# Kernel optimization log

Measured on AMD Instinct MI355X. Metric: run time of the kernel, lower is better.

The kernel has to match this reference:

```python
import jax, jax.numpy as jnp
import numpy as np

GROUPS = 4
BN_EPS = 1e-5


def conv2d(x, w, pad=0):
    return jax.lax.conv_general_dilated(x, w, (1, 1), [(pad, pad), (pad, pad)],
                                        dimension_numbers=('NCHW', 'OIHW', 'NCHW'))


def bn_infer(x, g, b, m, v):
    s = g * jax.lax.rsqrt(v + BN_EPS)
    return x * s[None, :, None, None] + (b - m * s)[None, :, None, None]


def refine_residual(x, w1, w3a, g, b, m, v, w3b):
    # RefineResidual(has_relu=True): 1x1 -> ConvBnRelu(3x3) -> 3x3 conv, residual, relu
    x1 = conv2d(x, w1)
    t = jax.nn.relu(bn_infer(conv2d(x1, w3a, pad=1), g, b, m, v))
    t = conv2d(t, w3b, pad=1)
    return jax.nn.relu(t + x1)


def grid_edges(H, W):
    # 4-connected pixel grid: right + down neighbors
    idx = np.arange(H * W).reshape(H, W)
    eu = np.concatenate([idx[:, :-1].ravel(), idx[:-1, :].ravel()]).astype(np.int32)
    ev = np.concatenate([idx[:, 1:].ravel(), idx[1:, :].ravel()]).astype(np.int32)
    return jnp.asarray(eu), jnp.asarray(ev)


def boruvka_mst(w, eu, ev, N):
    # Boruvka MST over the grid graph; returns bool mask over edges (N-1 True).
    E = w.shape[0]
    nodes = jnp.arange(N, dtype=jnp.int32)
    order = jnp.argsort(w).astype(jnp.int32)                  # edge ids by weight (unique ranks)
    rank = jnp.zeros(E, jnp.int32).at[order].set(jnp.arange(E, dtype=jnp.int32))
    BIG = jnp.int32(E)
    R = int(np.ceil(np.log2(max(N, 2)))) + 2

    def flatten(p):
        return jax.lax.fori_loop(0, R, lambda _, q: q[q], p)

    def body(_, state):
        parent, mst = state
        cu, cv = parent[eu], parent[ev]
        key = jnp.where(cu != cv, rank, BIG)
        cmin = jnp.minimum(jax.ops.segment_min(key, cu, num_segments=N),
                           jax.ops.segment_min(key, cv, num_segments=N))
        valid = cmin < BIG
        e = order[jnp.minimum(cmin, E - 1)]                   # min outgoing edge per component
        mst = mst.at[e].max(valid)
        other = jnp.where(cu[e] == nodes, cv[e], cu[e])
        pnew = jnp.where(valid, other, nodes)
        # break mutual (2-cycle) merges: smaller label becomes root
        pnew = jnp.where((pnew[pnew] == nodes) & (nodes < pnew), nodes, pnew)
        return flatten(pnew), mst

    _, mst = jax.lax.fori_loop(0, R + 2, body, (nodes, jnp.zeros(E, bool)))
    return mst


def root_and_depth(mst, eu, ev, N):
    # BFS-root the tree at node 0 -> parent pointers, then depth by pointer doubling.
    pn = jnp.full(N, -1, jnp.int32).at[0].set(0)

    def bfs(_, pn):
        vis = pn >= 0
        a = mst & vis[eu] & (~vis[ev])
        b = mst & vis[ev] & (~vis[eu])
        pn = pn.at[ev].max(jnp.where(a, eu, jnp.int32(-1)))
        pn = pn.at[eu].max(jnp.where(b, ev, jnp.int32(-1)))
        return pn

    pn = jax.lax.fori_loop(0, N, bfs, pn)
    R = int(np.ceil(np.log2(max(N, 2)))) + 2
    d0 = (jnp.arange(N) != 0).astype(jnp.int32)

    def dbl(_, s):
        d, p = s
        return d + d[p], p[p]

    depth, _ = jax.lax.fori_loop(0, R, dbl, (d0, pn))
    return pn, depth


def tree_filter_group(x, w, pn, depth):
    # Exact O(N) two-pass tree filter: y_i = sum_j prod(path weights i->j) x_j.
    # x: [N, C] (ones channel appended by caller), w: [N] edge weight to parent.
    N = x.shape[0]
    notroot = jnp.arange(N) != 0

    def up(i, agg):                                           # leaves -> root
        lev = N - 1 - i
        sel = (depth == lev) & notroot
        return agg.at[pn].add(jnp.where(sel[:, None], w[:, None] * agg, 0.0))

    agg = jax.lax.fori_loop(0, N - 1, up, x)

    def down(lev, F):                                         # root -> leaves
        cand = agg + w[:, None] * (F[pn] - w[:, None] * agg)
        return jnp.where(((depth == lev) & notroot)[:, None], cand, F)

    return jax.lax.fori_loop(1, N, down, agg)


def tree_filter_2d(feat, emb, pn, depth):
    # Grouped normalized tree filtering (TreeFilter2D): per-group edge affinity
    # exp(-||e_v - e_parent(v)||^2); normalize by filtering an all-ones channel.
    B, C, H, W = feat.shape
    N = H * W
    f = feat.reshape(B, GROUPS, C // GROUPS, N)
    e = emb.reshape(B, GROUPS, -1, N)

    def per_batch(fb, eb, pnb, db):
        w = jnp.exp(-jnp.sum((eb - eb[:, :, pnb]) ** 2, axis=1))   # [G, N]
        x = jnp.concatenate([fb, jnp.ones_like(fb[:, :1])], axis=1)
        x = jnp.swapaxes(x, 1, 2)                                  # [G, N, Cg+1]
        out = jax.vmap(lambda xg, wg: tree_filter_group(xg, wg, pnb, db))(x, w)
        y = out[..., :-1] / out[..., -1:]
        return jnp.swapaxes(y, 1, 2)

    out = jax.vmap(per_batch)(f, e, pn, depth)
    return out.reshape(B, C, H, W)


def _forward(fm, last_fm, lat_w1, lat_w3a, lat_g, lat_b, lat_m, lat_v, lat_w3b,
             ref_w1, ref_w3a, ref_g, ref_b, ref_m, ref_v, ref_w3b, emb_w):
    B, Cb, H, W = fm.shape
    N = H * W
    eu, ev = grid_edges(H, W)
    latent = refine_residual(fm, lat_w1, lat_w3a, lat_g, lat_b, lat_m, lat_v, lat_w3b)
    # MinimumSpanningTree(norm2_distance) on backbone features fm
    f = fm.reshape(B, Cb, N)
    dist = jnp.sum((f[:, :, eu] - f[:, :, ev]) ** 2, axis=1)       # [B, E]
    mst = jax.vmap(lambda d: boruvka_mst(d, eu, ev, N))(dist)
    pn, depth = jax.vmap(lambda m: root_and_depth(m, eu, ev, N))(mst)
    embed = conv2d(last_fm, emb_w)                                 # embed_layer (1x1, no bn/relu)
    fusion = latent + tree_filter_2d(last_fm, embed, pn, depth)
    return refine_residual(fusion, ref_w1, ref_w3a, ref_g, ref_b, ref_m, ref_v, ref_w3b)


def setup_inputs() -> dict:
    key = jax.random.key(0)
    ks = jax.random.split(key, 12)
    B, Cb, Cbiz, Cemb, H, W = 2, 1024, 64, 32, 32, 32
    r = lambda k, s: jax.random.normal(k, s, jnp.float32) * 0.05
    return dict(
        fm=jax.random.normal(ks[0], (B, Cb, H, W), jnp.float32),
        last_fm=jax.random.normal(ks[1], (B, Cbiz, H, W), jnp.float32),
        lat_w1=r(ks[2], (Cbiz, Cb, 1, 1)),
        lat_w3a=r(ks[3], (Cbiz, Cbiz, 3, 3)),
        lat_g=jnp.ones(Cbiz, jnp.float32),
        lat_b=jnp.zeros(Cbiz, jnp.float32),
        lat_m=jnp.zeros(Cbiz, jnp.float32),
        lat_v=jax.random.uniform(ks[4], (Cbiz,), jnp.float32, 0.5, 1.5),
        lat_w3b=r(ks[5], (Cbiz, Cbiz, 3, 3)),
        ref_w1=r(ks[6], (Cbiz, Cbiz, 1, 1)),
        ref_w3a=r(ks[7], (Cbiz, Cbiz, 3, 3)),
        ref_g=jnp.ones(Cbiz, jnp.float32),
        ref_b=jnp.zeros(Cbiz, jnp.float32),
        ref_m=jnp.zeros(Cbiz, jnp.float32),
        ref_v=jax.random.uniform(ks[8], (Cbiz,), jnp.float32, 0.5, 1.5),
        ref_w3b=r(ks[9], (Cbiz, Cbiz, 3, 3)),
        emb_w=r(ks[10], (Cemb, Cbiz, 1, 1)),
    )


def reference(fm, last_fm, lat_w1, lat_w3a, lat_g, lat_b, lat_m, lat_v, lat_w3b,
              ref_w1, ref_w3a, ref_g, ref_b, ref_m, ref_v, ref_w3b, emb_w):
    return _forward(fm, last_fm, lat_w1, lat_w3a, lat_g, lat_b, lat_m, lat_v, lat_w3b,
                    ref_w1, ref_w3a, ref_g, ref_b, ref_m, ref_v, ref_w3b, emb_w)
```

## Files before the change

kernel.cpp:

```cpp
#include <hip/hip_runtime.h>
#include <hip/hip_bf16.h>

#define NN 1024
#define EE 1984

__device__ __forceinline__ void edge_uv(int e, int* u, int* v) {
    if (e < 992) {
        int r = e / 31, c = e - r * 31;
        *u = r * 32 + c; *v = *u + 1;
    } else {
        *u = e - 992; *v = *u + 32;
    }
}

__device__ void conv1x1_tile(const float* __restrict__ in, const float* __restrict__ in2,
                             const float* __restrict__ w,
                             float* __restrict__ out, int CIN, int Cout,
                             int b, int co0, int n0, float* red) {
    int tid = threadIdx.x;
    int px = tid & 63, kc = tid >> 6;
    int kcu = __builtin_amdgcn_readfirstlane(kc);
    int KCH = CIN >> 4;
    size_t ibase = (size_t)b * CIN * NN + n0 + px;
    const float* wr = w + (size_t)co0 * CIN;
    float acc[8] = {0.f,0.f,0.f,0.f,0.f,0.f,0.f,0.f};
    for (int ci = kcu * KCH; ci < kcu * KCH + KCH; ++ci) {
        float xv = in[ibase + (size_t)ci * NN];
        if (in2) xv += in2[ibase + (size_t)ci * NN];
#pragma unroll
        for (int j = 0; j < 8; ++j)
            acc[j] += wr[j * CIN + ci] * xv;
    }
#pragma unroll
    for (int j = 0; j < 8; ++j) red[j * 1024 + tid] = acc[j];
    __syncthreads();
    for (int s = 8; s >= 1; s >>= 1) {
        if (kc < s) {
#pragma unroll
            for (int j = 0; j < 8; ++j)
                red[j * 1024 + kc * 64 + px] += red[j * 1024 + (kc + s) * 64 + px];
        }
        __syncthreads();
    }
    if (kc == 0) {
        size_t ob = ((size_t)b * Cout + co0) * NN + n0 + px;
#pragma unroll
        for (int j = 0; j < 8; ++j) out[ob + (size_t)j * NN] = red[j * 1024 + px];
    }
}

__device__ void dist_tile(const float* __restrict__ fm, float* __restrict__ dist,
                          int b, int eb, float* red) {
    int tid = threadIdx.x;
    int le = tid & 63, kc = tid >> 6;
    int kcu = __builtin_amdgcn_readfirstlane(kc);
    int e = eb * 64 + le;
    int u, v; edge_uv(e, &u, &v);
    const float* fp = fm + (size_t)b * 1024 * NN;
    float s = 0.f;
    for (int c = kcu * 64; c < kcu * 64 + 64; ++c) {
        float d = fp[(size_t)c * NN + u] - fp[(size_t)c * NN + v];
        s += d * d;
    }
    red[tid] = s;
    __syncthreads();
    for (int ss = 8; ss >= 1; ss >>= 1) {
        if (kc < ss) red[kc * 64 + le] += red[(kc + ss) * 64 + le];
        __syncthreads();
    }
    if (kc == 0) dist[b * EE + e] = red[le];
}

__device__ void conv3x3_body(const float* __restrict__ in, const float* __restrict__ w,
                             const float* __restrict__ gg, const float* __restrict__ bb,
                             const float* __restrict__ mm, const float* __restrict__ vv,
                             const float* __restrict__ res, float* __restrict__ out,
                             int mode, int b, int co, int r0, float* pl) {
    int tid = threadIdx.x;
    const float* ip = in + (size_t)b * 64 * NN;
    const float* wp = w + (size_t)co * 64 * 9;
    int r = tid >> 5, c = tid & 31;
    float acc = 0.f;
    for (int h = 0; h < 2; ++h) {
        __syncthreads();
        for (int i4 = tid; i4 < 32 * 80; i4 += 256) {
            int ci = i4 / 80, o = i4 - ci * 80;
            int row = r0 - 1 + (o >> 3), c4 = (o & 7) << 2;
            float4 val = make_float4(0.f, 0.f, 0.f, 0.f);
            if (row >= 0 && row < 32)
                val = *(const float4*)&ip[(size_t)(h * 32 + ci) * NN + row * 32 + c4];
            *(float4*)&pl[ci * 320 + (o >> 3) * 32 + c4] = val;
        }
        __syncthreads();
        for (int ci = 0; ci < 32; ++ci) {
            float wv[9];
#pragma unroll
            for (int q = 0; q < 9; ++q) wv[q] = wp[(h * 32 + ci) * 9 + q];
            float s = 0.f;
#pragma unroll
            for (int dy = 0; dy < 3; ++dy) {
                const float* row = &pl[ci * 320 + (r + dy) * 32];
#pragma unroll
                for (int dx = -1; dx <= 1; ++dx) {
                    int cc = c + dx;
                    float xv = (cc >= 0 && cc < 32) ? row[cc] : 0.f;
                    s += wv[dy * 3 + (dx + 1)] * xv;
                }
            }
            acc += s;
        }
    }
    float val;
    size_t op = ((size_t)b * 64 + co) * NN + r0 * 32 + tid;
    if (mode == 0) {
        float sc = gg[co] * rsqrtf(vv[co] + 1e-5f);
        val = acc * sc + (bb[co] - mm[co] * sc);
    } else {
        val = acc + res[op];
    }
    out[op] = fmaxf(val, 0.f);
}

struct MstS {
    unsigned long long minkey[NN];
    unsigned long long ekey[EE];
    int parent[NN], pnw[NN], pn[NN], dep[NN], scr[NN], elist[NN];
    int mstm[EE];
    int cnt, cnt2;
};

__device__ void mst_body_1024(const float* __restrict__ dist, int b, MstS* S,
                              int* __restrict__ pn_g, int* __restrict__ maxd_g,
                              int* __restrict__ ord_g, int* __restrict__ off_g) {
    int tid = threadIdx.x;
    const float* wb = dist + b * EE;
    S->parent[tid] = tid;
    for (int e = tid; e < EE; e += 1024) {
        S->mstm[e] = 0;
        S->ekey[e] = ((unsigned long long)__float_as_uint(wb[e]) << 32) | (unsigned)e;
    }
    if (tid == 0) { S->cnt = 0; S->cnt2 = 0; }
    __syncthreads();

    for (int round = 0; round < 14; ++round) {
        S->minkey[tid] = ~0ULL;
        __syncthreads();
        for (int e = tid; e < EE; e += 1024) {
            int u, v; edge_uv(e, &u, &v);
            int cu = S->parent[u], cv = S->parent[v];
            if (cu != cv) {
                unsigned long long k = S->ekey[e];
                atomicMin(&S->minkey[cu], k);
                atomicMin(&S->minkey[cv], k);
            }
        }
        __syncthreads();
        int np;
        unsigned long long mk = S->minkey[tid];
        if (mk != ~0ULL) {
            int e = (int)(mk & 0xffffffffULL);
            if (atomicExch(&S->mstm[e], 1) == 0) atomicAdd(&S->cnt, 1);
            int eu, ev; edge_uv(e, &eu, &ev);
            int cu = S->parent[eu], cv = S->parent[ev];
            np = (cu == tid) ? cv : cu;
        } else np = tid;
        S->pnw[tid] = np;
        __syncthreads();
        int q = S->pnw[tid];
        int pq = S->pnw[q];
        S->parent[tid] = (pq == tid && tid < q) ? tid : q;
        for (;;) {
            int ch = 0;
            int p = S->parent[tid];
            int pp = S->parent[p];
            if (pp != p) { S->parent[tid] = pp; ch = 1; }
            if (!__syncthreads_or(ch)) break;
        }
        if (S->cnt == NN - 1) break;
    }

    for (int e = tid; e < EE; e += 1024)
        if (S->mstm[e]) { int s = atomicAdd(&S->cnt2, 1); S->elist[s] = e; }
    __syncthreads();
    int ecnt = S->cnt2;

    S->pn[tid] = (tid == 0) ? 0 : -1;
    __syncthreads();
    volatile int* vpn = S->pn;
    int myu = 0, myv = 0; bool have = tid < ecnt;
    if (have) { edge_uv(S->elist[tid], &myu, &myv); }
    for (;;) {
        int ch = 0;
        for (int s = 0; s < 8; ++s) {
            if (have) {
                int pu = vpn[myu], pv = vpn[myv];
                if (pu >= 0 && pv < 0)      { vpn[myv] = myu; ch = 1; }
                else if (pv >= 0 && pu < 0) { vpn[myu] = myv; ch = 1; }
            }
        }
        if (!__syncthreads_or(ch)) break;
    }

    S->dep[tid] = (tid != 0) ? 1 : 0;
    S->pnw[tid] = S->pn[tid];
    __syncthreads();
    int* dA = S->dep; int* dB = S->scr; int* pA = S->pnw; int* pB = S->parent;
    for (int it = 0; it < 12; ++it) {
        int p = pA[tid];
        int j = (p < 0) ? (NN + p) : p;
        int nd = dA[tid] + dA[j];
        int np2 = pA[j];
        __syncthreads();
        dB[tid] = nd; pB[tid] = np2;
        __syncthreads();
        int* t = dA; dA = dB; dB = t;
        t = pA; pA = pB; pB = t;
    }
    if (tid == 0) S->cnt = 0;
    __syncthreads();
    int d = S->dep[tid];
    if (d >= 1 && d <= NN - 1) atomicMax(&S->cnt, d);
    __syncthreads();
    int maxd = S->cnt;

    S->scr[tid] = 0;
    __syncthreads();
    int bkt = (tid != 0 && d >= 1 && d <= NN - 1) ? d : 0;
    atomicAdd(&S->scr[bkt], 1);
    __syncthreads();
    int cntv = S->scr[tid];
    int lane = tid & 63, wid = tid >> 6;
    int x = cntv;
    for (int d2 = 1; d2 < 64; d2 <<= 1) {
        int y = __shfl_up(x, d2, 64);
        if (lane >= d2) x += y;
    }
    if (lane == 63) S->pnw[wid] = x;
    __syncthreads();
    if (tid < 16) {
        int off = 0;
        for (int i = 0; i < tid; ++i) off += S->pnw[i];
        S->parent[tid] = off;
    }
    __syncthreads();
    int excl = x - cntv + S->parent[wid];
    int* mi = (int*)S->minkey;
    mi[tid] = excl;
    S->scr[tid] = excl;
    __syncthreads();
    int pos = atomicAdd(&S->scr[bkt], 1);
    S->elist[pos] = tid;
    __syncthreads();

    pn_g[b * NN + tid]    = S->pn[tid];
    ord_g[b * NN + tid]   = S->elist[tid];
    off_g[b * 1025 + tid] = mi[tid];
    if (tid == 0) { off_g[b * 1025 + 1024] = NN; maxd_g[b] = maxd; }
}

struct TfSmem { float agg[NN * 3]; float wv[NN]; int jj[NN]; int ords[NN]; int offs[1025]; };
__device__ void treefilter_wave(const float* __restrict__ feat, const float* __restrict__ emb,
                                const int* __restrict__ pn_g, const int* __restrict__ ord_g,
                                const int* __restrict__ off_g, const int* __restrict__ maxd_g,
                                float* __restrict__ tfout, int b, int g, int sub, TfSmem* S) {
    int lane = threadIdx.x;
    const float* eb = emb + ((size_t)b * 32 + g * 8) * NN;
    int c0 = g * 16 + sub * 2;
    const float* fb = feat + ((size_t)b * 64 + c0) * NN;
    for (int k = 0; k < 16; ++k) {
        int v = lane + k * 64;
        int p = pn_g[b * NN + v];
        int j = (p < 0) ? (NN + p) : p;
        S->jj[v] = j;
        float s = 0.f;
#pragma unroll
        for (int q = 0; q < 8; ++q) {
            float d = eb[(size_t)q * NN + v] - eb[(size_t)q * NN + j];
            s += d * d;
        }
        S->wv[v] = expf(-s);
        S->agg[v * 3 + 0] = fb[v];
        S->agg[v * 3 + 1] = fb[NN + v];
        S->agg[v * 3 + 2] = 1.f;
        S->ords[v] = ord_g[b * NN + v];
        S->offs[v] = off_g[b * 1025 + v];
    }
    if (lane == 0) S->offs[1024] = NN;
    int maxdep = maxd_g[b];
    for (int lev = maxdep; lev >= 1; --lev) {
        int s0 = S->offs[lev], s1 = S->offs[lev + 1];
        for (int i = s0 + lane; i < s1; i += 64) {
            int v = S->ords[i]; int j = S->jj[v]; float w = S->wv[v];
            atomicAdd(&S->agg[j * 3 + 0], w * S->agg[v * 3 + 0]);
            atomicAdd(&S->agg[j * 3 + 1], w * S->agg[v * 3 + 1]);
            atomicAdd(&S->agg[j * 3 + 2], w * S->agg[v * 3 + 2]);
        }
    }
    for (int lev = 1; lev <= maxdep; ++lev) {
        int s0 = S->offs[lev], s1 = S->offs[lev + 1];
        for (int i = s0 + lane; i < s1; i += 64) {
            int v = S->ords[i]; int j = S->jj[v]; float w = S->wv[v];
#pragma unroll
            for (int c = 0; c < 3; ++c) {
                float a = S->agg[v * 3 + c];
                S->agg[v * 3 + c] = a + w * (S->agg[j * 3 + c] - w * a);
            }
        }
    }
    float* ob = tfout + ((size_t)b * 64 + c0) * NN;
    for (int k = 0; k < 16; ++k) {
        int v = lane + k * 64;
        float inv = 1.f / S->agg[v * 3 + 2];
        ob[v]      = S->agg[v * 3 + 0] * inv;
        ob[NN + v] = S->agg[v * 3 + 1] * inv;
    }
}

__global__ __launch_bounds__(1024) void k0_dist(
    const float* __restrict__ fm, float* __restrict__ dist) {
    __shared__ float red[1024];
    int i = blockIdx.x;
    dist_tile(fm, dist, i / 31, i % 31, red);
}

union K1S { float red[8192]; MstS m; };
__global__ __launch_bounds__(1024) void k1_fused(
    const float* __restrict__ fm, const float* __restrict__ last_fm,
    const float* __restrict__ lat_w1, const float* __restrict__ emb_w,
    float* __restrict__ lat_x1, float* __restrict__ embed,
    const float* __restrict__ dist, int* __restrict__ pn_g,
    int* __restrict__ maxd_g, int* __restrict__ ord_g, int* __restrict__ off_g) {
    __shared__ __align__(16) K1S s;
    int bx = blockIdx.x;
    if (bx < 2) {
        mst_body_1024(dist, bx, &s.m, pn_g, maxd_g, ord_g, off_g);
    } else if (bx < 258) {
        int i = bx - 2, b = i >> 7, r = i & 127;
        conv1x1_tile(fm, nullptr, lat_w1, lat_x1, 1024, 64,
                     b, (r >> 4) * 8, (r & 15) * 64, s.red);
    } else {
        int i = bx - 258, b = i >> 6, r = i & 63;
        conv1x1_tile(last_fm, nullptr, emb_w, embed, 64, 32,
                     b, (r >> 4) * 8, (r & 15) * 64, s.red);
    }
}

union K2S { float pl[32 * 320]; TfSmem t; };
__global__ __launch_bounds__(256) void k2_fused(
    const float* __restrict__ lat_x1, const float* __restrict__ lat_w3a,
    const float* __restrict__ lat_g, const float* __restrict__ lat_b,
    const float* __restrict__ lat_m, const float* __restrict__ lat_v,
    float* __restrict__ lat_t1,
    const float* __restrict__ last_fm, const float* __restrict__ embed,
    const int* __restrict__ pn_g, const int* __restrict__ ord_g,
    const int* __restrict__ off_g, const int* __restrict__ maxd_g,
    float* __restrict__ tfout) {
    __shared__ __align__(16) K2S s;
    int bx = blockIdx.x;
    if (bx < 64) {
        if (threadIdx.x >= 64) return;
        treefilter_wave(last_fm, embed, pn_g, ord_g, off_g, maxd_g, tfout,
                        bx >> 5, (bx >> 3) & 3, bx & 7, &s.t);
    } else {
        int i = bx - 64, b = i >> 8, co = (i >> 2) & 63, r0 = (i & 3) * 8;
        conv3x3_body(lat_x1, lat_w3a, lat_g, lat_b, lat_m, lat_v,
                     nullptr, lat_t1, 0, b, co, r0, s.pl);
    }
}

__global__ __launch_bounds__(256) void conv3x3_kernel(
    const float* __restrict__ in, const float* __restrict__ w,
    const float* __restrict__ gg, const float* __restrict__ bb,
    const float* __restrict__ mm, const float* __restrict__ vv,
    const float* __restrict__ res, float* __restrict__ out, int mode) {
    __shared__ __align__(16) float pl[32 * 320];
    conv3x3_body(in, w, gg, bb, mm, vv, res, out, mode,
                 blockIdx.z, blockIdx.y, blockIdx.x * 8, pl);
}

__global__ __launch_bounds__(1024) void conv1x1_add_kernel(
    const float* __restrict__ in, const float* __restrict__ in2,
    const float* __restrict__ w, float* __restrict__ out, int CIN, int Cout) {
    __shared__ float red[8192];
    conv1x1_tile(in, in2, w, out, CIN, Cout, blockIdx.z, blockIdx.y * 8,
                 blockIdx.x * 64, red);
}

extern "C" void kernel_launch(void* const* d_in, const int* in_sizes, int n_in,
                              void* d_out, int out_size, void* d_ws, size_t ws_size,
                              hipStream_t stream) {
    const float* fm      = (const float*)d_in[0];
    const float* last_fm = (const float*)d_in[1];
    const float* lat_w1  = (const float*)d_in[2];
    const float* lat_w3a = (const float*)d_in[3];
    const float* lat_g   = (const float*)d_in[4];
    const float* lat_b   = (const float*)d_in[5];
    const float* lat_m   = (const float*)d_in[6];
    const float* lat_v   = (const float*)d_in[7];
    const float* lat_w3b = (const float*)d_in[8];
    const float* ref_w1  = (const float*)d_in[9];
    const float* ref_w3a = (const float*)d_in[10];
    const float* ref_g   = (const float*)d_in[11];
    const float* ref_b   = (const float*)d_in[12];
    const float* ref_m   = (const float*)d_in[13];
    const float* ref_v   = (const float*)d_in[14];
    const float* ref_w3b = (const float*)d_in[15];
    const float* emb_w   = (const float*)d_in[16];
    float* out = (float*)d_out;

    float* ws      = (float*)d_ws;
    float* lat_x1  = ws;
    float* lat_t1  = lat_x1 + 131072;
    float* latent  = lat_t1 + 131072;
    float* dist    = latent + 131072;
    float* embed   = dist + 4096;
    float* tfout   = embed + 65536;
    float* ref_x1  = tfout + 131072;
    float* ref_t1  = ref_x1 + 131072;
    int*   pn      = (int*)(ref_t1 + 131072);
    int*   ordg    = pn + 2048;
    int*   offg    = ordg + 2048;
    int*   maxd    = offg + 2080;

    k0_dist<<<62, 1024, 0, stream>>>(fm, dist);
    k1_fused<<<386, 1024, 0, stream>>>(fm, last_fm, lat_w1, emb_w,
                                       lat_x1, embed, dist, pn, maxd, ordg, offg);
    k2_fused<<<576, 256, 0, stream>>>(lat_x1, lat_w3a, lat_g, lat_b, lat_m, lat_v,
                                      lat_t1, last_fm, embed, pn, ordg, offg,
                                      maxd, tfout);
    conv3x3_kernel<<<dim3(4, 64, 2), 256, 0, stream>>>(
        lat_t1, lat_w3b, nullptr, nullptr, nullptr, nullptr, lat_x1, latent, 1);
    conv1x1_add_kernel<<<dim3(16, 8, 2), 1024, 0, stream>>>(
        latent, tfout, ref_w1, ref_x1, 64, 64);
    conv3x3_kernel<<<dim3(4, 64, 2), 256, 0, stream>>>(
        ref_x1, ref_w3a, ref_g, ref_b, ref_m, ref_v, nullptr, ref_t1, 0);
    conv3x3_kernel<<<dim3(4, 64, 2), 256, 0, stream>>>(
        ref_t1, ref_w3b, nullptr, nullptr, nullptr, nullptr, ref_x1, out, 1);
}
```

Baseline: 243.6 us.

## Fuse all stages into one cooperative persistent kernel with grid syncs

Replaces the seven separate kernel launches with a single cooperative kernel of up to 256 blocks of 1024 threads that runs the stages in turn, separated by grid-wide barriers. The 3x3 conv is rewritten so one 1024-thread block computes a whole 32x32 output plane, staging 8 input channels at a time, instead of 256-thread blocks on 8-row strips. The aim is to cut launch and inter-kernel gaps. In exchange, the conv stages now have only 128 work items, so most blocks sit idle, and the single-block MST and tree-filter stages gate each barrier.

```diff
diff --git a/kernel.cpp b/kernel.cpp
--- a/kernel.cpp
+++ b/kernel.cpp
@@ -1,5 +1,8 @@
 #include <hip/hip_runtime.h>
 #include <hip/hip_bf16.h>
+#include <hip/hip_cooperative_groups.h>
+
+namespace cg = cooperative_groups;
 
 #define NN 1024
 #define EE 1984
@@ -71,47 +74,46 @@
     if (kc == 0) dist[b * EE + e] = red[le];
 }
 
-__device__ void conv3x3_body(const float* __restrict__ in, const float* __restrict__ w,
+__device__ void conv3x3_1024(const float* __restrict__ in, const float* __restrict__ w,
                              const float* __restrict__ gg, const float* __restrict__ bb,
                              const float* __restrict__ mm, const float* __restrict__ vv,
                              const float* __restrict__ res, float* __restrict__ out,
-                             int mode, int b, int co, int r0, float* pl) {
+                             int mode, int b, int co, float* pl) {
     int tid = threadIdx.x;
+    int r = tid >> 5, c = tid & 31;
     const float* ip = in + (size_t)b * 64 * NN;
     const float* wp = w + (size_t)co * 64 * 9;
-    int r = tid >> 5, c = tid & 31;
     float acc = 0.f;
-    for (int h = 0; h < 2; ++h) {
-        __syncthreads();
-        for (int i4 = tid; i4 < 32 * 80; i4 += 256) {
-            int ci = i4 / 80, o = i4 - ci * 80;
-            int row = r0 - 1 + (o >> 3), c4 = (o & 7) << 2;
-            float4 val = make_float4(0.f, 0.f, 0.f, 0.f);
-            if (row >= 0 && row < 32)
-                val = *(const float4*)&ip[(size_t)(h * 32 + ci) * NN + row * 32 + c4];
-            *(float4*)&pl[ci * 320 + (o >> 3) * 32 + c4] = val;
-        }
-        __syncthreads();
-        for (int ci = 0; ci < 32; ++ci) {
+    for (int h = 0; h < 8; ++h) {
+        __syncthreads();
+        for (int i4 = tid; i4 < 2048; i4 += 1024) {
+            int ci = i4 >> 8, o4 = (i4 & 255) << 2;
+            *(float4*)&pl[ci * 1024 + o4] =
+                *(const float4*)&ip[(size_t)(h * 8 + ci) * NN + o4];
+        }
+        __syncthreads();
+        for (int ci = 0; ci < 8; ++ci) {
             float wv[9];
 #pragma unroll
-            for (int q = 0; q < 9; ++q) wv[q] = wp[(h * 32 + ci) * 9 + q];
+            for (int q = 0; q < 9; ++q) wv[q] = wp[(h * 8 + ci) * 9 + q];
+            const float* P = &pl[ci * 1024];
             float s = 0.f;
 #pragma unroll
-            for (int dy = 0; dy < 3; ++dy) {
-                const float* row = &pl[ci * 320 + (r + dy) * 32];
+            for (int dy = -1; dy <= 1; ++dy) {
+                int rr = r + dy;
+                if (rr < 0 || rr >= 32) continue;
 #pragma unroll
                 for (int dx = -1; dx <= 1; ++dx) {
                     int cc = c + dx;
-                    float xv = (cc >= 0 && cc < 32) ? row[cc] : 0.f;
-                    s += wv[dy * 3 + (dx + 1)] * xv;
+                    float xv = (cc >= 0 && cc < 32) ? P[rr * 32 + cc] : 0.f;
+                    s += wv[(dy + 1) * 3 + (dx + 1)] * xv;
                 }
             }
             acc += s;
         }
     }
     float val;
-    size_t op = ((size_t)b * 64 + co) * NN + r0 * 32 + tid;
+    size_t op = ((size_t)b * 64 + co) * NN + tid;
     if (mode == 0) {
         float sc = gg[co] * rsqrtf(vv[co] + 1e-5f);
         val = acc * sc + (bb[co] - mm[co] * sc);
@@ -256,6 +258,7 @@
     ord_g[b * NN + tid]   = S->elist[tid];
     off_g[b * 1025 + tid] = mi[tid];
     if (tid == 0) { off_g[b * 1025 + 1024] = NN; maxd_g[b] = maxd; }
+    __threadfence();
 }
 
 struct TfSmem { float agg[NN * 3]; float wv[NN]; int jj[NN]; int ords[NN]; int offs[1025]; };
@@ -316,124 +319,137 @@
     }
 }
 
-__global__ __launch_bounds__(1024) void k0_dist(
-    const float* __restrict__ fm, float* __restrict__ dist) {
-    __shared__ float red[1024];
-    int i = blockIdx.x;
-    dist_tile(fm, dist, i / 31, i % 31, red);
-}
-
-union K1S { float red[8192]; MstS m; };
-__global__ __launch_bounds__(1024) void k1_fused(
-    const float* __restrict__ fm, const float* __restrict__ last_fm,
-    const float* __restrict__ lat_w1, const float* __restrict__ emb_w,
-    float* __restrict__ lat_x1, float* __restrict__ embed,
-    const float* __restrict__ dist, int* __restrict__ pn_g,
-    int* __restrict__ maxd_g, int* __restrict__ ord_g, int* __restrict__ off_g) {
-    __shared__ __align__(16) K1S s;
-    int bx = blockIdx.x;
+struct Params {
+    const float *fm, *last_fm;
+    const float *lat_w1, *lat_w3a, *lat_g, *lat_b, *lat_m, *lat_v, *lat_w3b;
+    const float *ref_w1, *ref_w3a, *ref_g, *ref_b, *ref_m, *ref_v, *ref_w3b, *emb_w;
+    float *lat_x1, *lat_t1, *latent, *dist, *embed, *tfout, *ref_x1, *ref_t1, *out;
+    int *pn, *ordg, *offg, *maxd;
+};
+
+union MegaS {
+    float red[8192];
+    float pl[8192];
+    MstS  m;
+    TfSmem t;
+};
+
+__global__ __launch_bounds__(1024, 4) void mega(Params P) {
+    cg::grid_group grid = cg::this_grid();
+    __shared__ __align__(16) MegaS s;
+    int nb = gridDim.x, bx = blockIdx.x;
+
+    for (int t = bx; t < 446; t += nb) {
+        if (t < 62) {
+            dist_tile(P.fm, P.dist, t / 31, t % 31, s.red);
+        } else if (t < 318) {
+            int i = t - 62, b = i >> 7, r = i & 127;
+            conv1x1_tile(P.fm, nullptr, P.lat_w1, P.lat_x1, 1024, 64,
+                         b, (r >> 4) * 8, (r & 15) * 64, s.red);
+        } else {
+            int i = t - 318, b = i >> 6, r = i & 63;
+            conv1x1_tile(P.last_fm, nullptr, P.emb_w, P.embed, 64, 32,
+                         b, (r >> 4) * 8, (r & 15) * 64, s.red);
+        }
+        __syncthreads();
+    }
+    __threadfence();
+    grid.sync();
+
     if (bx < 2) {
-        mst_body_1024(dist, bx, &s.m, pn_g, maxd_g, ord_g, off_g);
-    } else if (bx < 258) {
-        int i = bx - 2, b = i >> 7, r = i & 127;
-        conv1x1_tile(fm, nullptr, lat_w1, lat_x1, 1024, 64,
+        mst_body_1024(P.dist, bx, &s.m, P.pn, P.maxd, P.ordg, P.offg);
+    } else {
+        for (int t = bx - 2; t < 128; t += nb - 2) {
+            conv3x3_1024(P.lat_x1, P.lat_w3a, P.lat_g, P.lat_b, P.lat_m, P.lat_v,
+                         nullptr, P.lat_t1, 0, t >> 6, t & 63, s.pl);
+            __syncthreads();
+        }
+    }
+    __threadfence();
+    grid.sync();
+
+    if (bx < 64) {
+        if (threadIdx.x < 64)
+            treefilter_wave(P.last_fm, P.embed, P.pn, P.ordg, P.offg, P.maxd,
+                            P.tfout, bx >> 5, (bx >> 3) & 3, bx & 7, &s.t);
+    } else {
+        for (int t = bx - 64; t < 128; t += nb - 64) {
+            conv3x3_1024(P.lat_t1, P.lat_w3b, nullptr, nullptr, nullptr, nullptr,
+                         P.lat_x1, P.latent, 1, t >> 6, t & 63, s.pl);
+            __syncthreads();
+        }
+    }
+    __threadfence();
+    grid.sync();
+
+    for (int t = bx; t < 256; t += nb) {
+        int b = t >> 7, r = t & 127;
+        conv1x1_tile(P.latent, P.tfout, P.ref_w1, P.ref_x1, 64, 64,
                      b, (r >> 4) * 8, (r & 15) * 64, s.red);
-    } else {
-        int i = bx - 258, b = i >> 6, r = i & 63;
-        conv1x1_tile(last_fm, nullptr, emb_w, embed, 64, 32,
-                     b, (r >> 4) * 8, (r & 15) * 64, s.red);
-    }
-}
-
-union K2S { float pl[32 * 320]; TfSmem t; };
-__global__ __launch_bounds__(256) void k2_fused(
-    const float* __restrict__ lat_x1, const float* __restrict__ lat_w3a,
-    const float* __restrict__ lat_g, const float* __restrict__ lat_b,
-    const float* __restrict__ lat_m, const float* __restrict__ lat_v,
-    float* __restrict__ lat_t1,
-    const float* __restrict__ last_fm, const float* __restrict__ embed,
-    const int* __restrict__ pn_g, const int* __restrict__ ord_g,
-    const int* __restrict__ off_g, const int* __restrict__ maxd_g,
-    float* __restrict__ tfout) {
-    __shared__ __align__(16) K2S s;
-    int bx = blockIdx.x;
-    if (bx < 64) {
-        if (threadIdx.x >= 64) return;
-        treefilter_wave(last_fm, embed, pn_g, ord_g, off_g, maxd_g, tfout,
-                        bx >> 5, (bx >> 3) & 3, bx & 7, &s.t);
-    } else {
-        int i = bx - 64, b = i >> 8, co = (i >> 2) & 63, r0 = (i & 3) * 8;
-        conv3x3_body(lat_x1, lat_w3a, lat_g, lat_b, lat_m, lat_v,
-                     nullptr, lat_t1, 0, b, co, r0, s.pl);
-    }
-}
-
-__global__ __launch_bounds__(256) void conv3x3_kernel(
-    const float* __restrict__ in, const float* __restrict__ w,
-    const float* __restrict__ gg, const float* __restrict__ bb,
-    const float* __restrict__ mm, const float* __restrict__ vv,
-    const float* __restrict__ res, float* __restrict__ out, int mode) {
-    __shared__ __align__(16) float pl[32 * 320];
-    conv3x3_body(in, w, gg, bb, mm, vv, res, out, mode,
-                 blockIdx.z, blockIdx.y, blockIdx.x * 8, pl);
-}
-
-__global__ __launch_bounds__(1024) void conv1x1_add_kernel(
-    const float* __restrict__ in, const float* __restrict__ in2,
-    const float* __restrict__ w, float* __restrict__ out, int CIN, int Cout) {
-    __shared__ float red[8192];
-    conv1x1_tile(in, in2, w, out, CIN, Cout, blockIdx.z, blockIdx.y * 8,
-                 blockIdx.x * 64, red);
+        __syncthreads();
+    }
+    __threadfence();
+    grid.sync();
+
+    for (int t = bx; t < 128; t += nb) {
+        conv3x3_1024(P.ref_x1, P.ref_w3a, P.ref_g, P.ref_b, P.ref_m, P.ref_v,
+                     nullptr, P.ref_t1, 0, t >> 6, t & 63, s.pl);
+        __syncthreads();
+    }
+    __threadfence();
+    grid.sync();
+
+    for (int t = bx; t < 128; t += nb) {
+        conv3x3_1024(P.ref_t1, P.ref_w3b, nullptr, nullptr, nullptr, nullptr,
+                     P.ref_x1, P.out, 1, t >> 6, t & 63, s.pl);
+        __syncthreads();
+    }
 }
 
 extern "C" void kernel_launch(void* const* d_in, const int* in_sizes, int n_in,
                               void* d_out, int out_size, void* d_ws, size_t ws_size,
                               hipStream_t stream) {
-    const float* fm      = (const float*)d_in[0];
-    const float* last_fm = (const float*)d_in[1];
-    const float* lat_w1  = (const float*)d_in[2];
-    const float* lat_w3a = (const float*)d_in[3];
-    const float* lat_g   = (const float*)d_in[4];
-    const float* lat_b   = (const float*)d_in[5];
-    const float* lat_m   = (const float*)d_in[6];
-    const float* lat_v   = (const float*)d_in[7];
-    const float* lat_w3b = (const float*)d_in[8];
-    const float* ref_w1  = (const float*)d_in[9];
-    const float* ref_w3a = (const float*)d_in[10];
-    const float* ref_g   = (const float*)d_in[11];
-    const float* ref_b   = (const float*)d_in[12];
-    const float* ref_m   = (const float*)d_in[13];
-    const float* ref_v   = (const float*)d_in[14];
-    const float* ref_w3b = (const float*)d_in[15];
-    const float* emb_w   = (const float*)d_in[16];
-    float* out = (float*)d_out;
-
-    float* ws      = (float*)d_ws;
-    float* lat_x1  = ws;
-    float* lat_t1  = lat_x1 + 131072;
-    float* latent  = lat_t1 + 131072;
-    float* dist    = latent + 131072;
-    float* embed   = dist + 4096;
-    float* tfout   = embed + 65536;
-    float* ref_x1  = tfout + 131072;
-    float* ref_t1  = ref_x1 + 131072;
-    int*   pn      = (int*)(ref_t1 + 131072);
-    int*   ordg    = pn + 2048;
-    int*   offg    = ordg + 2048;
-    int*   maxd    = offg + 2080;
-
-    k0_dist<<<62, 1024, 0, stream>>>(fm, dist);
-    k1_fused<<<386, 1024, 0, stream>>>(fm, last_fm, lat_w1, emb_w,
-                                       lat_x1, embed, dist, pn, maxd, ordg, offg);
-    k2_fused<<<576, 256, 0, stream>>>(lat_x1, lat_w3a, lat_g, lat_b, lat_m, lat_v,
-                                      lat_t1, last_fm, embed, pn, ordg, offg,
-                                      maxd, tfout);
-    conv3x3_kernel<<<dim3(4, 64, 2), 256, 0, stream>>>(
-        lat_t1, lat_w3b, nullptr, nullptr, nullptr, nullptr, lat_x1, latent, 1);
-    conv1x1_add_kernel<<<dim3(16, 8, 2), 1024, 0, stream>>>(
-        latent, tfout, ref_w1, ref_x1, 64, 64);
-    conv3x3_kernel<<<dim3(4, 64, 2), 256, 0, stream>>>(
-        ref_x1, ref_w3a, ref_g, ref_b, ref_m, ref_v, nullptr, ref_t1, 0);
-    conv3x3_kernel<<<dim3(4, 64, 2), 256, 0, stream>>>(
-        ref_t1, ref_w3b, nullptr, nullptr, nullptr, nullptr, ref_x1, out, 1);
-}
+    Params P;
+    P.fm      = (const float*)d_in[0];
+    P.last_fm = (const float*)d_in[1];
+    P.lat_w1  = (const float*)d_in[2];
+    P.lat_w3a = (const float*)d_in[3];
+    P.lat_g   = (const float*)d_in[4];
+    P.lat_b   = (const float*)d_in[5];
+    P.lat_m   = (const float*)d_in[6];
+    P.lat_v   = (const float*)d_in[7];
+    P.lat_w3b = (const float*)d_in[8];
+    P.ref_w1  = (const float*)d_in[9];
+    P.ref_w3a = (const float*)d_in[10];
+    P.ref_g   = (const float*)d_in[11];
+    P.ref_b   = (const float*)d_in[12];
+    P.ref_m   = (const float*)d_in[13];
+    P.ref_v   = (const float*)d_in[14];
+    P.ref_w3b = (const float*)d_in[15];
+    P.emb_w   = (const float*)d_in[16];
+    P.out     = (float*)d_out;
+
+    float* ws  = (float*)d_ws;
+    P.lat_x1   = ws;
+    P.lat_t1   = P.lat_x1 + 131072;
+    P.latent   = P.lat_t1 + 131072;
+    P.dist     = P.latent + 131072;
+    P.embed    = P.dist + 4096;
+    P.tfout    = P.embed + 65536;
+    P.ref_x1   = P.tfout + 131072;
+    P.ref_t1   = P.ref_x1 + 131072;
+    P.pn       = (int*)(P.ref_t1 + 131072);
+    P.ordg     = P.pn + 2048;
+    P.offg     = P.ordg + 2048;
+    P.maxd     = P.offg + 2080;
+
+    int occ = 0;
+    hipOccupancyMaxActiveBlocksPerMultiprocessor(&occ, mega, 1024, 0);
+    if (occ < 1) occ = 1;
+    int grid = 256 * occ;
+    if (grid > 256) grid = 256;
+
+    void* args[] = { &P };
+    hipLaunchCooperativeKernel((const void*)mega, dim3(grid), dim3(1024),
+                               args, 0, stream);
+}
```

Result: slower. 680.8 us (+179.5%).

## Restructure kernel schedule to overlap MST and treefilter with whole-plane 3x3 convs

Applied to the files above, without the earlier changes.

Splits the stages across launches differently. Distance computation and both 1x1 convs now share the first launch. The MST runs next to the first 3x3 conv, and the tree filter runs next to the second lateral 3x3 conv. The result is six launches instead of seven, and the serial MST and tree-filter blocks are hidden behind parallel conv work. The 3x3 conv is rewritten so each 1024-thread block computes a full 32x32 output plane, loading 8 input channels per stage without halo rows. The MST loop drops one barrier per round and runs more propagation steps per sync. The trade-off is fewer blocks per conv (128 instead of 512), which lowers parallelism, and larger blocks with more shared memory.

```diff
diff --git a/kernel.cpp b/kernel.cpp
--- a/kernel.cpp
+++ b/kernel.cpp
@@ -71,47 +71,46 @@
     if (kc == 0) dist[b * EE + e] = red[le];
 }
 
-__device__ void conv3x3_body(const float* __restrict__ in, const float* __restrict__ w,
+__device__ void conv3x3_1024(const float* __restrict__ in, const float* __restrict__ w,
                              const float* __restrict__ gg, const float* __restrict__ bb,
                              const float* __restrict__ mm, const float* __restrict__ vv,
                              const float* __restrict__ res, float* __restrict__ out,
-                             int mode, int b, int co, int r0, float* pl) {
+                             int mode, int b, int co, float* pl) {
     int tid = threadIdx.x;
+    int r = tid >> 5, c = tid & 31;
     const float* ip = in + (size_t)b * 64 * NN;
     const float* wp = w + (size_t)co * 64 * 9;
-    int r = tid >> 5, c = tid & 31;
     float acc = 0.f;
-    for (int h = 0; h < 2; ++h) {
-        __syncthreads();
-        for (int i4 = tid; i4 < 32 * 80; i4 += 256) {
-            int ci = i4 / 80, o = i4 - ci * 80;
-            int row = r0 - 1 + (o >> 3), c4 = (o & 7) << 2;
-            float4 val = make_float4(0.f, 0.f, 0.f, 0.f);
-            if (row >= 0 && row < 32)
-                val = *(const float4*)&ip[(size_t)(h * 32 + ci) * NN + row * 32 + c4];
-            *(float4*)&pl[ci * 320 + (o >> 3) * 32 + c4] = val;
-        }
-        __syncthreads();
-        for (int ci = 0; ci < 32; ++ci) {
+    for (int h = 0; h < 8; ++h) {
+        __syncthreads();
+        for (int i4 = tid; i4 < 2048; i4 += 1024) {
+            int ci = i4 >> 8, o4 = (i4 & 255) << 2;
+            *(float4*)&pl[ci * 1024 + o4] =
+                *(const float4*)&ip[(size_t)(h * 8 + ci) * NN + o4];
+        }
+        __syncthreads();
+        for (int ci = 0; ci < 8; ++ci) {
             float wv[9];
 #pragma unroll
-            for (int q = 0; q < 9; ++q) wv[q] = wp[(h * 32 + ci) * 9 + q];
+            for (int q = 0; q < 9; ++q) wv[q] = wp[(h * 8 + ci) * 9 + q];
+            const float* P = &pl[ci * 1024];
             float s = 0.f;
 #pragma unroll
-            for (int dy = 0; dy < 3; ++dy) {
-                const float* row = &pl[ci * 320 + (r + dy) * 32];
+            for (int dy = -1; dy <= 1; ++dy) {
+                int rr = r + dy;
+                if (rr < 0 || rr >= 32) continue;
 #pragma unroll
                 for (int dx = -1; dx <= 1; ++dx) {
                     int cc = c + dx;
-                    float xv = (cc >= 0 && cc < 32) ? row[cc] : 0.f;
-                    s += wv[dy * 3 + (dx + 1)] * xv;
+                    float xv = (cc >= 0 && cc < 32) ? P[rr * 32 + cc] : 0.f;
+                    s += wv[(dy + 1) * 3 + (dx + 1)] * xv;
                 }
             }
             acc += s;
         }
     }
     float val;
-    size_t op = ((size_t)b * 64 + co) * NN + r0 * 32 + tid;
+    size_t op = ((size_t)b * 64 + co) * NN + tid;
     if (mode == 0) {
         float sc = gg[co] * rsqrtf(vv[co] + 1e-5f);
         val = acc * sc + (bb[co] - mm[co] * sc);
@@ -135,6 +134,7 @@
     int tid = threadIdx.x;
     const float* wb = dist + b * EE;
     S->parent[tid] = tid;
+    S->minkey[tid] = ~0ULL;
     for (int e = tid; e < EE; e += 1024) {
         S->mstm[e] = 0;
         S->ekey[e] = ((unsigned long long)__float_as_uint(wb[e]) << 32) | (unsigned)e;
@@ -143,8 +143,6 @@
     __syncthreads();
 
     for (int round = 0; round < 14; ++round) {
-        S->minkey[tid] = ~0ULL;
-        __syncthreads();
         for (int e = tid; e < EE; e += 1024) {
             int u, v; edge_uv(e, &u, &v);
             int cu = S->parent[u], cv = S->parent[v];
@@ -157,6 +155,7 @@
         __syncthreads();
         int np;
         unsigned long long mk = S->minkey[tid];
+        S->minkey[tid] = ~0ULL;
         if (mk != ~0ULL) {
             int e = (int)(mk & 0xffffffffULL);
             if (atomicExch(&S->mstm[e], 1) == 0) atomicAdd(&S->cnt, 1);
@@ -191,7 +190,7 @@
     if (have) { edge_uv(S->elist[tid], &myu, &myv); }
     for (;;) {
         int ch = 0;
-        for (int s = 0; s < 8; ++s) {
+        for (int s = 0; s < 16; ++s) {
             if (have) {
                 int pu = vpn[myu], pv = vpn[myv];
                 if (pu >= 0 && pv < 0)      { vpn[myv] = myu; ch = 1; }
@@ -316,74 +315,82 @@
     }
 }
 
-__global__ __launch_bounds__(1024) void k0_dist(
-    const float* __restrict__ fm, float* __restrict__ dist) {
-    __shared__ float red[1024];
-    int i = blockIdx.x;
-    dist_tile(fm, dist, i / 31, i % 31, red);
-}
-
-union K1S { float red[8192]; MstS m; };
-__global__ __launch_bounds__(1024) void k1_fused(
+__global__ __launch_bounds__(1024) void k0_fused(
     const float* __restrict__ fm, const float* __restrict__ last_fm,
     const float* __restrict__ lat_w1, const float* __restrict__ emb_w,
-    float* __restrict__ lat_x1, float* __restrict__ embed,
+    float* __restrict__ lat_x1, float* __restrict__ embed, float* __restrict__ dist) {
+    __shared__ __align__(16) float red[8192];
+    int bx = blockIdx.x;
+    if (bx < 62) {
+        dist_tile(fm, dist, bx / 31, bx % 31, red);
+    } else if (bx < 318) {
+        int i = bx - 62, b = i >> 7, r = i & 127;
+        conv1x1_tile(fm, nullptr, lat_w1, lat_x1, 1024, 64,
+                     b, (r >> 4) * 8, (r & 15) * 64, red);
+    } else {
+        int i = bx - 318, b = i >> 6, r = i & 63;
+        conv1x1_tile(last_fm, nullptr, emb_w, embed, 64, 32,
+                     b, (r >> 4) * 8, (r & 15) * 64, red);
+    }
+}
+
+union K1S { float pl[8192]; MstS m; };
+__global__ __launch_bounds__(1024) void k1_fused(
     const float* __restrict__ dist, int* __restrict__ pn_g,
-    int* __restrict__ maxd_g, int* __restrict__ ord_g, int* __restrict__ off_g) {
+    int* __restrict__ maxd_g, int* __restrict__ ord_g, int* __restrict__ off_g,
+    const float* __restrict__ lat_x1, const float* __restrict__ lat_w3a,
+    const float* __restrict__ lat_g, const float* __restrict__ lat_b,
+    const float* __restrict__ lat_m, const float* __restrict__ lat_v,
+    float* __restrict__ lat_t1) {
     __shared__ __align__(16) K1S s;
     int bx = blockIdx.x;
     if (bx < 2) {
         mst_body_1024(dist, bx, &s.m, pn_g, maxd_g, ord_g, off_g);
-    } else if (bx < 258) {
-        int i = bx - 2, b = i >> 7, r = i & 127;
-        conv1x1_tile(fm, nullptr, lat_w1, lat_x1, 1024, 64,
-                     b, (r >> 4) * 8, (r & 15) * 64, s.red);
     } else {
-        int i = bx - 258, b = i >> 6, r = i & 63;
-        conv1x1_tile(last_fm, nullptr, emb_w, embed, 64, 32,
-                     b, (r >> 4) * 8, (r & 15) * 64, s.red);
-    }
-}
-
-union K2S { float pl[32 * 320]; TfSmem t; };
-__global__ __launch_bounds__(256) void k2_fused(
-    const float* __restrict__ lat_x1, const float* __restrict__ lat_w3a,
-    const float* __restrict__ lat_g, const float* __restrict__ lat_b,
-    const float* __restrict__ lat_m, const float* __restrict__ lat_v,
-    float* __restrict__ lat_t1,
+        int t = bx - 2;
+        conv3x3_1024(lat_x1, lat_w3a, lat_g, lat_b, lat_m, lat_v,
+                     nullptr, lat_t1, 0, t >> 6, t & 63, s.pl);
+    }
+}
+
+union K2S { float pl[8192]; TfSmem t; };
+__global__ __launch_bounds__(1024) void k2_fused(
     const float* __restrict__ last_fm, const float* __restrict__ embed,
     const int* __restrict__ pn_g, const int* __restrict__ ord_g,
     const int* __restrict__ off_g, const int* __restrict__ maxd_g,
-    float* __restrict__ tfout) {
+    float* __restrict__ tfout,
+    const float* __restrict__ lat_t1, const float* __restrict__ lat_w3b,
+    const float* __restrict__ lat_x1, float* __restrict__ latent) {
     __shared__ __align__(16) K2S s;
     int bx = blockIdx.x;
     if (bx < 64) {
-        if (threadIdx.x >= 64) return;
-        treefilter_wave(last_fm, embed, pn_g, ord_g, off_g, maxd_g, tfout,
-                        bx >> 5, (bx >> 3) & 3, bx & 7, &s.t);
+        if (threadIdx.x < 64)
+            treefilter_wave(last_fm, embed, pn_g, ord_g, off_g, maxd_g, tfout,
+                            bx >> 5, (bx >> 3) & 3, bx & 7, &s.t);
     } else {
-        int i = bx - 64, b = i >> 8, co = (i >> 2) & 63, r0 = (i & 3) * 8;
-        conv3x3_body(lat_x1, lat_w3a, lat_g, lat_b, lat_m, lat_v,
-                     nullptr, lat_t1, 0, b, co, r0, s.pl);
-    }
-}
-
-__global__ __launch_bounds__(256) void conv3x3_kernel(
+        int t = bx - 64;
+        conv3x3_1024(lat_t1, lat_w3b, nullptr, nullptr, nullptr, nullptr,
+                     lat_x1, latent, 1, t >> 6, t & 63, s.pl);
+    }
+}
+
+__global__ __launch_bounds__(1024) void conv1x1_add_kernel(
+    const float* __restrict__ in, const float* __restrict__ in2,
+    const float* __restrict__ w, float* __restrict__ out, int CIN, int Cout) {
+    __shared__ float red[8192];
+    int bx = blockIdx.x;
+    int b = bx >> 7, r = bx & 127;
+    conv1x1_tile(in, in2, w, out, CIN, Cout, b, (r >> 4) * 8, (r & 15) * 64, red);
+}
+
+__global__ __launch_bounds__(1024) void conv3x3_tail(
     const float* __restrict__ in, const float* __restrict__ w,
     const float* __restrict__ gg, const float* __restrict__ bb,
     const float* __restrict__ mm, const float* __restrict__ vv,
     const float* __restrict__ res, float* __restrict__ out, int mode) {
-    __shared__ __align__(16) float pl[32 * 320];
-    conv3x3_body(in, w, gg, bb, mm, vv, res, out, mode,
-                 blockIdx.z, blockIdx.y, blockIdx.x * 8, pl);
-}
-
-__global__ __launch_bounds__(1024) void conv1x1_add_kernel(
-    const float* __restrict__ in, const float* __restrict__ in2,
-    const float* __restrict__ w, float* __restrict__ out, int CIN, int Cout) {
-    __shared__ float red[8192];
-    conv1x1_tile(in, in2, w, out, CIN, Cout, blockIdx.z, blockIdx.y * 8,
-                 blockIdx.x * 64, red);
+    __shared__ __align__(16) float pl[8192];
+    int t = blockIdx.x;
+    conv3x3_1024(in, w, gg, bb, mm, vv, res, out, mode, t >> 6, t & 63, pl);
 }
 
 extern "C" void kernel_launch(void* const* d_in, const int* in_sizes, int n_in,
@@ -422,18 +429,16 @@
     int*   offg    = ordg + 2048;
     int*   maxd    = offg + 2080;
 
-    k0_dist<<<62, 1024, 0, stream>>>(fm, dist);
-    k1_fused<<<386, 1024, 0, stream>>>(fm, last_fm, lat_w1, emb_w,
-                                       lat_x1, embed, dist, pn, maxd, ordg, offg);
-    k2_fused<<<576, 256, 0, stream>>>(lat_x1, lat_w3a, lat_g, lat_b, lat_m, lat_v,
-                                      lat_t1, last_fm, embed, pn, ordg, offg,
-                                      maxd, tfout);
-    conv3x3_kernel<<<dim3(4, 64, 2), 256, 0, stream>>>(
-        lat_t1, lat_w3b, nullptr, nullptr, nullptr, nullptr, lat_x1, latent, 1);
-    conv1x1_add_kernel<<<dim3(16, 8, 2), 1024, 0, stream>>>(
-        latent, tfout, ref_w1, ref_x1, 64, 64);
-    conv3x3_kernel<<<dim3(4, 64, 2), 256, 0, stream>>>(
-        ref_x1, ref_w3a, ref_g, ref_b, ref_m, ref_v, nullptr, ref_t1, 0);
-    conv3x3_kernel<<<dim3(4, 64, 2), 256, 0, stream>>>(
-        ref_t1, ref_w3b, nullptr, nullptr, nullptr, nullptr, ref_x1, out, 1);
-}
+    k0_fused<<<446, 1024, 0, stream>>>(fm, last_fm, lat_w1, emb_w,
+                                       lat_x1, embed, dist);
+    k1_fused<<<130, 1024, 0, stream>>>(dist, pn, maxd, ordg, offg,
+                                       lat_x1, lat_w3a, lat_g, lat_b, lat_m, lat_v,
+                                       lat_t1);
+    k2_fused<<<192, 1024, 0, stream>>>(last_fm, embed, pn, ordg, offg, maxd,
+                                       tfout, lat_t1, lat_w3b, lat_x1, latent);
+    conv1x1_add_kernel<<<256, 1024, 0, stream>>>(latent, tfout, ref_w1, ref_x1, 64, 64);
+    conv3x3_tail<<<128, 1024, 0, stream>>>(ref_x1, ref_w3a, ref_g, ref_b,
+                                           ref_m, ref_v, nullptr, ref_t1, 0);
+    conv3x3_tail<<<128, 1024, 0, stream>>>(ref_t1, ref_w3b, nullptr, nullptr,
+                                           nullptr, nullptr, ref_x1, out, 1);
+}
```

New measurement: 285.0 us. +17.0%, slower.

## Switch Boruvka min-edge search to per-node gather and trim barriers

Applied to the files above, without the earlier changes.

The Boruvka min-edge search now runs per node instead of per edge. Each thread looks at its four grid neighbours, takes the minimum key locally, and does one atomicMin into its component slot. That halves the shared-memory atomics and removes one barrier per round, because minkey is reset right after it is read. The pointer-jumping loop drops a barrier by using its double buffers directly, and the tree-propagation inner sweep goes from 8 to 16 steps per barrier check. The cost is more redundant per-thread work per sync, and correctness now depends on the reset-after-read ordering being safe across rounds.

```diff
diff --git a/kernel.cpp b/kernel.cpp
--- a/kernel.cpp
+++ b/kernel.cpp
@@ -135,6 +135,7 @@
     int tid = threadIdx.x;
     const float* wb = dist + b * EE;
     S->parent[tid] = tid;
+    S->minkey[tid] = ~0ULL;
     for (int e = tid; e < EE; e += 1024) {
         S->mstm[e] = 0;
         S->ekey[e] = ((unsigned long long)__float_as_uint(wb[e]) << 32) | (unsigned)e;
@@ -142,23 +143,33 @@
     if (tid == 0) { S->cnt = 0; S->cnt2 = 0; }
     __syncthreads();
 
+    int r = tid >> 5, c = tid & 31;
     for (int round = 0; round < 14; ++round) {
+        int pv = S->parent[tid];
+        unsigned long long mk = ~0ULL;
+        if (c < 31 && S->parent[tid + 1] != pv) {
+            unsigned long long k = S->ekey[r * 31 + c];
+            if (k < mk) mk = k;
+        }
+        if (c > 0 && S->parent[tid - 1] != pv) {
+            unsigned long long k = S->ekey[r * 31 + c - 1];
+            if (k < mk) mk = k;
+        }
+        if (r < 31 && S->parent[tid + 32] != pv) {
+            unsigned long long k = S->ekey[992 + r * 32 + c];
+            if (k < mk) mk = k;
+        }
+        if (r > 0 && S->parent[tid - 32] != pv) {
+            unsigned long long k = S->ekey[992 + (r - 1) * 32 + c];
+            if (k < mk) mk = k;
+        }
+        if (mk != ~0ULL) atomicMin(&S->minkey[pv], mk);
+        __syncthreads();
+        int np;
+        unsigned long long sel = S->minkey[tid];
         S->minkey[tid] = ~0ULL;
-        __syncthreads();
-        for (int e = tid; e < EE; e += 1024) {
-            int u, v; edge_uv(e, &u, &v);
-            int cu = S->parent[u], cv = S->parent[v];
-            if (cu != cv) {
-                unsigned long long k = S->ekey[e];
-                atomicMin(&S->minkey[cu], k);
-                atomicMin(&S->minkey[cv], k);
-            }
-        }
-        __syncthreads();
-        int np;
-        unsigned long long mk = S->minkey[tid];
-        if (mk != ~0ULL) {
-            int e = (int)(mk & 0xffffffffULL);
+        if (sel != ~0ULL) {
+            int e = (int)(sel & 0xffffffffULL);
             if (atomicExch(&S->mstm[e], 1) == 0) atomicAdd(&S->cnt, 1);
             int eu, ev; edge_uv(e, &eu, &ev);
             int cu = S->parent[eu], cv = S->parent[ev];
@@ -191,7 +202,7 @@
     if (have) { edge_uv(S->elist[tid], &myu, &myv); }
     for (;;) {
         int ch = 0;
-        for (int s = 0; s < 8; ++s) {
+        for (int s = 0; s < 16; ++s) {
             if (have) {
                 int pu = vpn[myu], pv = vpn[myv];
                 if (pu >= 0 && pv < 0)      { vpn[myv] = myu; ch = 1; }
@@ -208,10 +219,8 @@
     for (int it = 0; it < 12; ++it) {
         int p = pA[tid];
         int j = (p < 0) ? (NN + p) : p;
-        int nd = dA[tid] + dA[j];
-        int np2 = pA[j];
-        __syncthreads();
-        dB[tid] = nd; pB[tid] = np2;
+        dB[tid] = dA[tid] + dA[j];
+        pB[tid] = pA[j];
         __syncthreads();
         int* t = dA; dA = dB; dB = t;
         t = pA; pA = pB; pB = t;
```

Result: no change. 241.0 us (-1.1%).
